# Kernel optimization log

Hardware: AMD Instinct MI355X
Metric: run time of the kernel (lower is better)

## Reference

```python
import jax, jax.numpy as jnp
import numpy as np

NUM_HEADS = 8
NUM_LEVELS = 4
NUM_POINTS = 4
EMBED = 256
HEAD_DIM = EMBED // NUM_HEADS
SPATIAL = [(100, 100), (50, 50), (25, 25), (13, 13)]  # (H, W) per level


def _bilinear_sample(val, grid):
    """torch.nn.functional.grid_sample(mode='bilinear', padding_mode='zeros', align_corners=False).
    val: [B, H, W, C], grid: [B, N, 2] with (x, y) in [-1, 1]. Returns [B, N, C]."""
    B, H, W, C = val.shape
    x = (grid[..., 0] + 1.0) * (W * 0.5) - 0.5
    y = (grid[..., 1] + 1.0) * (H * 0.5) - 0.5
    x0 = jnp.floor(x)
    y0 = jnp.floor(y)
    wx1 = x - x0
    wy1 = y - y0
    wx0 = 1.0 - wx1
    wy0 = 1.0 - wy1
    x0i = x0.astype(jnp.int32)
    y0i = y0.astype(jnp.int32)
    valf = val.reshape(B, H * W, C)

    def corner(xi, yi, w):
        valid = (xi >= 0) & (xi < W) & (yi >= 0) & (yi < H)
        idx = jnp.clip(yi, 0, H - 1) * W + jnp.clip(xi, 0, W - 1)
        v = jnp.take_along_axis(valf, idx[..., None], axis=1)  # [B, N, C]
        return v * (w * valid)[..., None]

    return (corner(x0i, y0i, wx0 * wy0) + corner(x0i + 1, y0i, wx1 * wy0)
            + corner(x0i, y0i + 1, wx0 * wy1) + corner(x0i + 1, y0i + 1, wx1 * wy1))


def setup_inputs() -> dict:
    key = jax.random.key(0)
    ks = jax.random.split(key, 12)
    bs, nq = 4, 6000
    nv = sum(h * w for h, w in SPATIAL)
    s = 0.02
    return {
        "query": jax.random.normal(ks[0], (bs, nq, EMBED), jnp.float32),
        "value": jax.random.normal(ks[1], (bs, nv, EMBED), jnp.float32),
        "reference_points": jax.random.uniform(ks[2], (bs, nq, NUM_LEVELS, 2), jnp.float32),
        "W_off": jax.random.normal(ks[3], (EMBED, NUM_HEADS * NUM_LEVELS * NUM_POINTS * 2), jnp.float32) * s,
        "b_off": jax.random.normal(ks[4], (NUM_HEADS * NUM_LEVELS * NUM_POINTS * 2,), jnp.float32),
        "W_attn": jax.random.normal(ks[5], (EMBED, NUM_HEADS * NUM_LEVELS * NUM_POINTS), jnp.float32) * s,
        "b_attn": jnp.zeros((NUM_HEADS * NUM_LEVELS * NUM_POINTS,), jnp.float32),
        "W_val": jax.random.normal(ks[6], (EMBED, EMBED), jnp.float32) * s,
        "b_val": jnp.zeros((EMBED,), jnp.float32),
        "W_out": jax.random.normal(ks[7], (EMBED, EMBED), jnp.float32) * s,
        "b_out": jnp.zeros((EMBED,), jnp.float32),
        "spatial_shapes": jnp.asarray(np.array(SPATIAL, dtype=np.int32)),
    }


def reference(query, value, reference_points, W_off, b_off, W_attn, b_attn,
              W_val, b_val, W_out, b_out, spatial_shapes):
    shapes = [(int(h), int(w)) for h, w in np.asarray(spatial_shapes)]
    bs, nq, _ = query.shape
    nv = value.shape[1]

    v = (value @ W_val + b_val).reshape(bs, nv, NUM_HEADS, HEAD_DIM)
    offsets = (query @ W_off + b_off).reshape(bs, nq, NUM_HEADS, NUM_LEVELS, NUM_POINTS, 2)
    aw = (query @ W_attn + b_attn).reshape(bs, nq, NUM_HEADS, NUM_LEVELS * NUM_POINTS)
    aw = jax.nn.softmax(aw, axis=-1).reshape(bs, nq, NUM_HEADS, NUM_LEVELS, NUM_POINTS)

    # offset normalizer is [W, H] per level
    norm = jnp.asarray([[w, h] for h, w in shapes], dtype=query.dtype)  # [L, 2]
    loc = reference_points[:, :, None, :, None, :] + offsets / norm[None, None, None, :, None, :]
    grids = 2.0 * loc - 1.0  # [bs, nq, H, L, P, 2]
    # -> [bs*H, nq*P, 2] per level
    grids = jnp.transpose(grids, (0, 2, 1, 3, 4, 5)).reshape(bs * NUM_HEADS, nq, NUM_LEVELS, NUM_POINTS, 2)

    v_bh = jnp.transpose(v, (0, 2, 1, 3)).reshape(bs * NUM_HEADS, nv, HEAD_DIM)
    sampled = []
    start = 0
    for l, (H_, W_) in enumerate(shapes):
        val_l = v_bh[:, start:start + H_ * W_].reshape(bs * NUM_HEADS, H_, W_, HEAD_DIM)
        grid_l = grids[:, :, l].reshape(bs * NUM_HEADS, nq * NUM_POINTS, 2)
        s_l = _bilinear_sample(val_l, grid_l).reshape(bs * NUM_HEADS, nq, NUM_POINTS, HEAD_DIM)
        sampled.append(s_l)
        start += H_ * W_
    sampled = jnp.stack(sampled, axis=2)  # [bs*H, nq, L, P, c]

    aw_bh = jnp.transpose(aw, (0, 2, 1, 3, 4)).reshape(bs * NUM_HEADS, nq, NUM_LEVELS, NUM_POINTS)
    out = (sampled * aw_bh[..., None]).sum(axis=(2, 3))  # [bs*H, nq, c]
    out = out.reshape(bs, NUM_HEADS, nq, HEAD_DIM).transpose(0, 2, 1, 3).reshape(bs, nq, EMBED)
    out = out @ W_out + b_out
    return out + query
```

## Files before the change

kernel.cpp:

```cpp
#include <hip/hip_runtime.h>
#include <hip/hip_bf16.h>

#define BS 4
#define NQ 6000
#define NV 13294
#define NH 8
#define HD 32
#define EMB 256
#define MV (BS * NV)
#define MQ (BS * NQ)

typedef __attribute__((ext_vector_type(8))) short short8;
typedef __attribute__((ext_vector_type(4))) float floatx4;

__device__ __constant__ float LVL_DIM[4] = {100.f, 50.f, 25.f, 13.f};

__device__ inline unsigned short bf16bits(float f) {
  __hip_bfloat16 h = __float2bfloat16(f);
  return *reinterpret_cast<unsigned short*>(&h);
}
__device__ inline float bflo(unsigned int u) { return __uint_as_float(u << 16); }
__device__ inline float bfhi(unsigned int u) { return __uint_as_float(u & 0xffff0000u); }

#define LDS_STRIDE 40

__global__ __launch_bounds__(256) void wtrans_kernel(
    const float* __restrict__ W_val, const float* __restrict__ W_off,
    const float* __restrict__ W_attn, const float* __restrict__ W_out,
    unsigned short* __restrict__ Wt_val, unsigned short* __restrict__ Wt_qcat,
    unsigned short* __restrict__ Wt_out) {
  const int b = blockIdx.x, k = threadIdx.x;
  if (b < 256) {
    Wt_val[b * EMB + k] = bf16bits(W_val[k * 256 + b]);
  } else if (b < 640) {
    const int n = b - 256;
    float v = (n < 256) ? W_off[k * 256 + n] : W_attn[k * 128 + (n - 256)];
    Wt_qcat[n * EMB + k] = bf16bits(v);
  } else {
    const int n = b - 640;
    Wt_out[n * EMB + k] = bf16bits(W_out[k * 256 + n]);
  }
}

__device__ inline void stageA_f32(const float* __restrict__ A, int M, int m0,
                                  int k0, unsigned short* lds, int tid) {
  const int r = tid >> 1, half = tid & 1;
  const int row = m0 + r;
  unsigned short* dst = lds + r * LDS_STRIDE + half * 16;
  if (row < M) {
    const float* src = A + (size_t)row * EMB + k0 + half * 16;
#pragma unroll
    for (int j = 0; j < 4; ++j) {
      float4 v = *(const float4*)(src + 4 * j);
      ushort4 u;
      u.x = bf16bits(v.x);
      u.y = bf16bits(v.y);
      u.z = bf16bits(v.z);
      u.w = bf16bits(v.w);
      *(ushort4*)(dst + 4 * j) = u;
    }
  } else {
    ushort4 z = make_ushort4(0, 0, 0, 0);
#pragma unroll
    for (int j = 0; j < 4; ++j) *(ushort4*)(dst + 4 * j) = z;
  }
}

__device__ inline void stage_bf16(const unsigned short* __restrict__ B, int M,
                                  int n0, int k0, unsigned short* lds, int tid) {
  const int r = tid >> 1, half = tid & 1;
  const int row = n0 + r;
  unsigned short* dst = lds + r * LDS_STRIDE + half * 16;
  if (row < M) {
    const unsigned short* src = B + (size_t)row * EMB + k0 + half * 16;
    uint4 v0 = *(const uint4*)(src);
    uint4 v1 = *(const uint4*)(src + 8);
    *(uint4*)(dst) = v0;
    *(uint4*)(dst + 8) = v1;
  } else {
    uint4 z = make_uint4(0, 0, 0, 0);
    *(uint4*)(dst) = z;
    *(uint4*)(dst + 8) = z;
  }
}

__device__ inline void mfma_step(const unsigned short* ldsA,
                                 const unsigned short* ldsB, int wm, int wn,
                                 int lane, floatx4 acc[4][4]) {
  const unsigned short* ap =
      ldsA + (wm * 64 + (lane & 15)) * LDS_STRIDE + (lane >> 4) * 8;
  const unsigned short* bp =
      ldsB + (wn * 64 + (lane & 15)) * LDS_STRIDE + (lane >> 4) * 8;
  short8 af[4], bfr[4];
#pragma unroll
  for (int t = 0; t < 4; ++t) {
    af[t] = *(const short8*)(ap + t * 16 * LDS_STRIDE);
    bfr[t] = *(const short8*)(bp + t * 16 * LDS_STRIDE);
  }
#pragma unroll
  for (int mt = 0; mt < 4; ++mt)
#pragma unroll
    for (int nt = 0; nt < 4; ++nt)
      acc[mt][nt] = __builtin_amdgcn_mfma_f32_16x16x32_bf16(af[mt], bfr[nt],
                                                            acc[mt][nt], 0, 0, 0);
}

__global__ __launch_bounds__(256) void vproj_kernel(
    const float* __restrict__ value, const unsigned short* __restrict__ Wt,
    const float* __restrict__ b_val, unsigned short* __restrict__ vbh) {
  __shared__ unsigned short ldsA[128 * LDS_STRIDE];
  __shared__ unsigned short ldsB[128 * LDS_STRIDE];
  const int tid = threadIdx.x, lane = tid & 63, w = tid >> 6;
  const int wm = w >> 1, wn = w & 1;
  const int m0 = (blockIdx.x >> 1) * 128;
  const int n0 = (blockIdx.x & 1) * 128;
  floatx4 acc[4][4];
  const floatx4 zero = {0.f, 0.f, 0.f, 0.f};
#pragma unroll
  for (int i = 0; i < 4; i++)
#pragma unroll
    for (int j = 0; j < 4; j++) acc[i][j] = zero;

  for (int k0 = 0; k0 < EMB; k0 += 32) {
    stageA_f32(value, MV, m0, k0, ldsA, tid);
    stage_bf16(Wt, 256, n0, k0, ldsB, tid);
    __syncthreads();
    mfma_step(ldsA, ldsB, wm, wn, lane, acc);
    __syncthreads();
  }

  const int quad = lane >> 4, cl = lane & 15;
#pragma unroll
  for (int mt = 0; mt < 4; ++mt) {
#pragma unroll
    for (int r = 0; r < 4; ++r) {
      const int row = m0 + wm * 64 + mt * 16 + quad * 4 + r;
      if (row < MV) {
        const int b = row / NV, n = row - b * NV;
#pragma unroll
        for (int nt = 0; nt < 4; ++nt) {
          const int c = n0 + wn * 64 + nt * 16 + cl;
          const int h = c >> 5, d = c & 31;
          vbh[(((size_t)(b * NH + h)) * NV + n) * HD + d] =
              bf16bits(acc[mt][nt][r] + b_val[c]);
        }
      }
    }
  }
}

__global__ __launch_bounds__(256) void qproj_kernel(
    const float* __restrict__ query, const unsigned short* __restrict__ Wt,
    const float* __restrict__ refpts, const float* __restrict__ b_off,
    const float* __restrict__ b_attn, float* __restrict__ locbuf,
    float* __restrict__ awbuf) {
  __shared__ unsigned short ldsA[128 * LDS_STRIDE];
  __shared__ unsigned short ldsB[128 * LDS_STRIDE];
  const int tid = threadIdx.x, lane = tid & 63, w = tid >> 6;
  const int wm = w >> 1, wn = w & 1;
  const int m0 = (blockIdx.x / 3) * 128;
  const int n0 = (blockIdx.x % 3) * 128;
  floatx4 acc[4][4];
  const floatx4 zero = {0.f, 0.f, 0.f, 0.f};
#pragma unroll
  for (int i = 0; i < 4; i++)
#pragma unroll
    for (int j = 0; j < 4; j++) acc[i][j] = zero;

  for (int k0 = 0; k0 < EMB; k0 += 32) {
    stageA_f32(query, MQ, m0, k0, ldsA, tid);
    stage_bf16(Wt, 384, n0, k0, ldsB, tid);
    __syncthreads();
    mfma_step(ldsA, ldsB, wm, wn, lane, acc);
    __syncthreads();
  }

  const int quad = lane >> 4, cl = lane & 15;
  if (n0 < 256) {
#pragma unroll
    for (int mt = 0; mt < 4; ++mt) {
#pragma unroll
      for (int r = 0; r < 4; ++r) {
        const int row = m0 + wm * 64 + mt * 16 + quad * 4 + r;
        if (row < MQ) {
#pragma unroll
          for (int nt = 0; nt < 4; ++nt) {
            const int c = n0 + wn * 64 + nt * 16 + cl;
            const int xy = c & 1, l = (c >> 3) & 3;
            const float dim = LVL_DIM[l];
            const float ref = refpts[(size_t)row * 8 + l * 2 + xy];
            locbuf[(size_t)row * 256 + c] =
                ref * dim + acc[mt][nt][r] + b_off[c] - 0.5f;
          }
        }
      }
    }
  } else {
#pragma unroll
    for (int mt = 0; mt < 4; ++mt) {
#pragma unroll
      for (int r = 0; r < 4; ++r) {
        const int row = m0 + wm * 64 + mt * 16 + quad * 4 + r;
        if (row < MQ) {
#pragma unroll
          for (int nt = 0; nt < 4; ++nt) {
            const int ca = wn * 64 + nt * 16 + cl;
            float v = acc[mt][nt][r] + b_attn[ca];
            float m = v;
            m = fmaxf(m, __shfl_xor(m, 1));
            m = fmaxf(m, __shfl_xor(m, 2));
            m = fmaxf(m, __shfl_xor(m, 4));
            m = fmaxf(m, __shfl_xor(m, 8));
            float e = __expf(v - m);
            float s = e;
            s += __shfl_xor(s, 1);
            s += __shfl_xor(s, 2);
            s += __shfl_xor(s, 4);
            s += __shfl_xor(s, 8);
            awbuf[(size_t)row * 128 + ca] = e / s;
          }
        }
      }
    }
  }
}

__global__ __launch_bounds__(256) void sample_kernel(
    const unsigned short* __restrict__ vbh, const float* __restrict__ locbuf,
    const float* __restrict__ awbuf, unsigned short* __restrict__ sampledb) {
  const int wid = (blockIdx.x * 256 + threadIdx.x) >> 6;
  const int lane = threadIdx.x & 63;
  const int h = wid & 7;
  const int row = wid >> 3;
  const int b = row / NQ;
  const unsigned int* vb =
      (const unsigned int*)(vbh) + ((size_t)(b * NH + h)) * NV * 16;
  const int grp = lane >> 4;
  const int d2 = lane & 15;

  const float* locp = locbuf + (size_t)row * 256 + h * 32;
  const float* awp = awbuf + (size_t)row * 128 + h * 16;

  float ax = 0.f, ay = 0.f;
#pragma unroll
  for (int l = 0; l < 4; ++l) {
    const int W_ = (l == 0) ? 100 : (l == 1) ? 50 : (l == 2) ? 25 : 13;
    const int H_ = W_;
    const int START = (l == 0) ? 0 : (l == 1) ? 10000 : (l == 2) ? 12500 : 13125;
    const int s = l * 4 + grp;
    const float2 xy = *(const float2*)(locp + s * 2);
    const float w = awp[s];

    const float fx = floorf(xy.x), fy = floorf(xy.y);
    const int x0 = (int)fx, y0 = (int)fy;
    const float wx1 = xy.x - fx, wy1 = xy.y - fy;
    const float wx0 = 1.f - wx1, wy0 = 1.f - wy1;

    const int x0c = min(max(x0, 0), W_ - 1), x1c = min(max(x0 + 1, 0), W_ - 1);
    const int y0c = min(max(y0, 0), H_ - 1), y1c = min(max(y0 + 1, 0), H_ - 1);
    const float mx0 = (x0 >= 0 && x0 < W_) ? wx0 : 0.f;
    const float mx1 = (x0 + 1 >= 0 && x0 + 1 < W_) ? wx1 : 0.f;
    const float my0 = (y0 >= 0 && y0 < H_) ? wy0 : 0.f;
    const float my1 = (y0 + 1 >= 0 && y0 + 1 < H_) ? wy1 : 0.f;

    const unsigned int* basep = vb + (size_t)START * 16 + d2;
    unsigned int u00 = basep[(y0c * W_ + x0c) * 16];
    unsigned int u01 = basep[(y0c * W_ + x1c) * 16];
    unsigned int u10 = basep[(y1c * W_ + x0c) * 16];
    unsigned int u11 = basep[(y1c * W_ + x1c) * 16];

    const float w00 = w * my0 * mx0, w01 = w * my0 * mx1;
    const float w10 = w * my1 * mx0, w11 = w * my1 * mx1;
    ax += w00 * bflo(u00) + w01 * bflo(u01) + w10 * bflo(u10) + w11 * bflo(u11);
    ay += w00 * bfhi(u00) + w01 * bfhi(u01) + w10 * bfhi(u10) + w11 * bfhi(u11);
  }
  ax += __shfl_xor(ax, 16);
  ax += __shfl_xor(ax, 32);
  ay += __shfl_xor(ay, 16);
  ay += __shfl_xor(ay, 32);
  if (grp == 0) {
    ushort2 o;
    o.x = bf16bits(ax);
    o.y = bf16bits(ay);
    *(ushort2*)(sampledb + (size_t)row * EMB + h * HD + 2 * d2) = o;
  }
}

__global__ __launch_bounds__(256) void oproj_kernel(
    const unsigned short* __restrict__ sampledb,
    const unsigned short* __restrict__ Wt, const float* __restrict__ b_out,
    const float* __restrict__ query, float* __restrict__ out) {
  __shared__ unsigned short ldsA[128 * LDS_STRIDE];
  __shared__ unsigned short ldsB[128 * LDS_STRIDE];
  const int tid = threadIdx.x, lane = tid & 63, w = tid >> 6;
  const int wm = w >> 1, wn = w & 1;
  const int m0 = (blockIdx.x >> 1) * 128;
  const int n0 = (blockIdx.x & 1) * 128;
  floatx4 acc[4][4];
  const floatx4 zero = {0.f, 0.f, 0.f, 0.f};
#pragma unroll
  for (int i = 0; i < 4; i++)
#pragma unroll
    for (int j = 0; j < 4; j++) acc[i][j] = zero;

  for (int k0 = 0; k0 < EMB; k0 += 32) {
    stage_bf16(sampledb, MQ, m0, k0, ldsA, tid);
    stage_bf16(Wt, 256, n0, k0, ldsB, tid);
    __syncthreads();
    mfma_step(ldsA, ldsB, wm, wn, lane, acc);
    __syncthreads();
  }

  const int quad = lane >> 4, cl = lane & 15;
#pragma unroll
  for (int mt = 0; mt < 4; ++mt) {
#pragma unroll
    for (int r = 0; r < 4; ++r) {
      const int row = m0 + wm * 64 + mt * 16 + quad * 4 + r;
      if (row < MQ) {
#pragma unroll
        for (int nt = 0; nt < 4; ++nt) {
          const int c = n0 + wn * 64 + nt * 16 + cl;
          out[(size_t)row * EMB + c] =
              acc[mt][nt][r] + b_out[c] + query[(size_t)row * EMB + c];
        }
      }
    }
  }
}

extern "C" void kernel_launch(void* const* d_in, const int* in_sizes, int n_in,
                              void* d_out, int out_size, void* d_ws,
                              size_t ws_size, hipStream_t stream) {
  const float* query  = (const float*)d_in[0];
  const float* value  = (const float*)d_in[1];
  const float* refpts = (const float*)d_in[2];
  const float* W_off  = (const float*)d_in[3];
  const float* b_off  = (const float*)d_in[4];
  const float* W_attn = (const float*)d_in[5];
  const float* b_attn = (const float*)d_in[6];
  const float* W_val  = (const float*)d_in[7];
  const float* b_val  = (const float*)d_in[8];
  const float* W_out  = (const float*)d_in[9];
  const float* b_out  = (const float*)d_in[10];
  float* out = (float*)d_out;

  char* ws = (char*)d_ws;
  unsigned short* vbh = (unsigned short*)ws;
  float* locbuf = (float*)(ws + 27226112);
  float* awbuf = (float*)(ws + 51802112);
  unsigned short* sampledb = (unsigned short*)(ws + 64090112);
  unsigned short* Wt_val = (unsigned short*)(ws + 76378112);
  unsigned short* Wt_qcat = (unsigned short*)(ws + 76509184);
  unsigned short* Wt_out = (unsigned short*)(ws + 76705792);

  wtrans_kernel<<<896, 256, 0, stream>>>(W_val, W_off, W_attn, W_out, Wt_val,
                                         Wt_qcat, Wt_out);
  vproj_kernel<<<416 * 2, 256, 0, stream>>>(value, Wt_val, b_val, vbh);
  qproj_kernel<<<188 * 3, 256, 0, stream>>>(query, Wt_qcat, refpts, b_off,
                                            b_attn, locbuf, awbuf);
  sample_kernel<<<BS * NQ * NH / 4, 256, 0, stream>>>(vbh, locbuf, awbuf,
                                                      sampledb);
  oproj_kernel<<<188 * 2, 256, 0, stream>>>(sampledb, Wt_out, b_out, query, out);
}
```

Measured before the change: 282.7 us.

## Remap GEMM block order per XCD and vectorize sampling with slice-grouped blocks

The three GEMM kernels now map block IDs so that blocks landing on the same XCD (blockIdx mod 8) share M tiles, which is meant to improve L2 reuse of the A operand. The sample kernel is restructured so each lane handles one sampling point and loads 8 bf16 channels as a uint4, replacing 4 scalar loads per point. It reduces across points with a shuffle tree. Blocks are also ordered so that each XCD works on a fixed set of (batch, head) value slices, keeping the gathered value slice resident in its L2. The cost is more shuffle instructions per wave and padded grids with early-exit blocks in qproj and oproj.

```diff
diff --git a/kernel.cpp b/kernel.cpp
--- a/kernel.cpp
+++ b/kernel.cpp
@@ -112,14 +112,15 @@
   __shared__ unsigned short ldsB[128 * LDS_STRIDE];
   const int tid = threadIdx.x, lane = tid & 63, w = tid >> 6;
   const int wm = w >> 1, wn = w & 1;
-  const int m0 = (blockIdx.x >> 1) * 128;
-  const int n0 = (blockIdx.x & 1) * 128;
+  const int chunk = blockIdx.x >> 4, i = blockIdx.x & 15;
+  const int m0 = (chunk * 8 + (i & 7)) * 128;
+  const int n0 = (i >> 3) * 128;
   floatx4 acc[4][4];
   const floatx4 zero = {0.f, 0.f, 0.f, 0.f};
 #pragma unroll
-  for (int i = 0; i < 4; i++)
-#pragma unroll
-    for (int j = 0; j < 4; j++) acc[i][j] = zero;
+  for (int i2 = 0; i2 < 4; i2++)
+#pragma unroll
+    for (int j = 0; j < 4; j++) acc[i2][j] = zero;
 
   for (int k0 = 0; k0 < EMB; k0 += 32) {
     stageA_f32(value, MV, m0, k0, ldsA, tid);
@@ -158,14 +159,17 @@
   __shared__ unsigned short ldsB[128 * LDS_STRIDE];
   const int tid = threadIdx.x, lane = tid & 63, w = tid >> 6;
   const int wm = w >> 1, wn = w & 1;
-  const int m0 = (blockIdx.x / 3) * 128;
-  const int n0 = (blockIdx.x % 3) * 128;
+  const int chunk = blockIdx.x / 24, i = blockIdx.x % 24;
+  const int m_idx = chunk * 8 + (i & 7);
+  if (m_idx >= 188) return;
+  const int m0 = m_idx * 128;
+  const int n0 = (i >> 3) * 128;
   floatx4 acc[4][4];
   const floatx4 zero = {0.f, 0.f, 0.f, 0.f};
 #pragma unroll
-  for (int i = 0; i < 4; i++)
-#pragma unroll
-    for (int j = 0; j < 4; j++) acc[i][j] = zero;
+  for (int i2 = 0; i2 < 4; i2++)
+#pragma unroll
+    for (int j = 0; j < 4; j++) acc[i2][j] = zero;
 
   for (int k0 = 0; k0 < EMB; k0 += 32) {
     stageA_f32(query, MQ, m0, k0, ldsA, tid);
@@ -228,61 +232,75 @@
 __global__ __launch_bounds__(256) void sample_kernel(
     const unsigned short* __restrict__ vbh, const float* __restrict__ locbuf,
     const float* __restrict__ awbuf, unsigned short* __restrict__ sampledb) {
-  const int wid = (blockIdx.x * 256 + threadIdx.x) >> 6;
+  const int blk = blockIdx.x;
+  const int t = blk >> 3;
+  const int quarter = t / 1500;
+  const int j = t - quarter * 1500;
+  const int slice = (blk & 7) * 4 + quarter;
+  const int h = slice & 7;
+  const int w = threadIdx.x >> 6;
   const int lane = threadIdx.x & 63;
-  const int h = wid & 7;
-  const int row = wid >> 3;
-  const int b = row / NQ;
-  const unsigned int* vb =
-      (const unsigned int*)(vbh) + ((size_t)(b * NH + h)) * NV * 16;
-  const int grp = lane >> 4;
-  const int d2 = lane & 15;
-
-  const float* locp = locbuf + (size_t)row * 256 + h * 32;
-  const float* awp = awbuf + (size_t)row * 128 + h * 16;
-
-  float ax = 0.f, ay = 0.f;
-#pragma unroll
-  for (int l = 0; l < 4; ++l) {
-    const int W_ = (l == 0) ? 100 : (l == 1) ? 50 : (l == 2) ? 25 : 13;
-    const int H_ = W_;
-    const int START = (l == 0) ? 0 : (l == 1) ? 10000 : (l == 2) ? 12500 : 13125;
-    const int s = l * 4 + grp;
-    const float2 xy = *(const float2*)(locp + s * 2);
-    const float w = awp[s];
-
-    const float fx = floorf(xy.x), fy = floorf(xy.y);
-    const int x0 = (int)fx, y0 = (int)fy;
-    const float wx1 = xy.x - fx, wy1 = xy.y - fy;
-    const float wx0 = 1.f - wx1, wy0 = 1.f - wy1;
-
-    const int x0c = min(max(x0, 0), W_ - 1), x1c = min(max(x0 + 1, 0), W_ - 1);
-    const int y0c = min(max(y0, 0), H_ - 1), y1c = min(max(y0 + 1, 0), H_ - 1);
-    const float mx0 = (x0 >= 0 && x0 < W_) ? wx0 : 0.f;
-    const float mx1 = (x0 + 1 >= 0 && x0 + 1 < W_) ? wx1 : 0.f;
-    const float my0 = (y0 >= 0 && y0 < H_) ? wy0 : 0.f;
-    const float my1 = (y0 + 1 >= 0 && y0 + 1 < H_) ? wy1 : 0.f;
-
-    const unsigned int* basep = vb + (size_t)START * 16 + d2;
-    unsigned int u00 = basep[(y0c * W_ + x0c) * 16];
-    unsigned int u01 = basep[(y0c * W_ + x1c) * 16];
-    unsigned int u10 = basep[(y1c * W_ + x0c) * 16];
-    unsigned int u11 = basep[(y1c * W_ + x1c) * 16];
-
-    const float w00 = w * my0 * mx0, w01 = w * my0 * mx1;
-    const float w10 = w * my1 * mx0, w11 = w * my1 * mx1;
-    ax += w00 * bflo(u00) + w01 * bflo(u01) + w10 * bflo(u10) + w11 * bflo(u11);
-    ay += w00 * bfhi(u00) + w01 * bfhi(u01) + w10 * bfhi(u10) + w11 * bfhi(u11);
-  }
-  ax += __shfl_xor(ax, 16);
-  ax += __shfl_xor(ax, 32);
-  ay += __shfl_xor(ay, 16);
-  ay += __shfl_xor(ay, 32);
-  if (grp == 0) {
-    ushort2 o;
-    o.x = bf16bits(ax);
-    o.y = bf16bits(ay);
-    *(ushort2*)(sampledb + (size_t)row * EMB + h * HD + 2 * d2) = o;
+  const int row = (slice >> 3) * NQ + j * 4 + w;
+  const int g = lane >> 2;
+  const int d8 = lane & 3;
+  const int l = g >> 2;
+
+  const int W_ = (l < 2) ? ((l == 0) ? 100 : 50) : ((l == 2) ? 25 : 13);
+  const int START = (l < 2) ? ((l == 0) ? 0 : 10000) : ((l == 2) ? 12500 : 13125);
+
+  const float2 xy = *(const float2*)(locbuf + (size_t)row * 256 + h * 32 + g * 2);
+  const float wgt = awbuf[(size_t)row * 128 + h * 16 + g];
+
+  const float fx = floorf(xy.x), fy = floorf(xy.y);
+  const int x0 = (int)fx, y0 = (int)fy;
+  const float wx1 = xy.x - fx, wy1 = xy.y - fy;
+  const float wx0 = 1.f - wx1, wy0 = 1.f - wy1;
+  const int x0c = min(max(x0, 0), W_ - 1), x1c = min(max(x0 + 1, 0), W_ - 1);
+  const int y0c = min(max(y0, 0), W_ - 1), y1c = min(max(y0 + 1, 0), W_ - 1);
+  const float mx0 = ((unsigned)x0 < (unsigned)W_) ? wx0 : 0.f;
+  const float mx1 = ((unsigned)(x0 + 1) < (unsigned)W_) ? wx1 : 0.f;
+  const float my0 = ((unsigned)y0 < (unsigned)W_) ? wy0 : 0.f;
+  const float my1 = ((unsigned)(y0 + 1) < (unsigned)W_) ? wy1 : 0.f;
+  const float wy0w = wgt * my0, wy1w = wgt * my1;
+  const float w00 = wy0w * mx0, w01 = wy0w * mx1;
+  const float w10 = wy1w * mx0, w11 = wy1w * mx1;
+
+  const unsigned int* base =
+      (const unsigned int*)vbh + ((size_t)slice * NV + START) * 16 + d8 * 4;
+  const int rb0 = y0c * W_, rb1 = y1c * W_;
+  const uint4 u00 = *(const uint4*)(base + (size_t)(rb0 + x0c) * 16);
+  const uint4 u01 = *(const uint4*)(base + (size_t)(rb0 + x1c) * 16);
+  const uint4 u10 = *(const uint4*)(base + (size_t)(rb1 + x0c) * 16);
+  const uint4 u11 = *(const uint4*)(base + (size_t)(rb1 + x1c) * 16);
+
+  float a[8];
+  const unsigned int* p00 = &u00.x;
+  const unsigned int* p01 = &u01.x;
+  const unsigned int* p10 = &u10.x;
+  const unsigned int* p11 = &u11.x;
+#pragma unroll
+  for (int k = 0; k < 4; ++k) {
+    a[2 * k] = w00 * bflo(p00[k]) + w01 * bflo(p01[k]) + w10 * bflo(p10[k]) +
+               w11 * bflo(p11[k]);
+    a[2 * k + 1] = w00 * bfhi(p00[k]) + w01 * bfhi(p01[k]) +
+                   w10 * bfhi(p10[k]) + w11 * bfhi(p11[k]);
+  }
+
+#pragma unroll
+  for (int k = 0; k < 8; ++k) {
+    a[k] += __shfl_xor(a[k], 4);
+    a[k] += __shfl_xor(a[k], 8);
+    a[k] += __shfl_xor(a[k], 16);
+    a[k] += __shfl_xor(a[k], 32);
+  }
+
+  if (g == 0) {
+    uint4 o;
+    o.x = (unsigned)bf16bits(a[0]) | ((unsigned)bf16bits(a[1]) << 16);
+    o.y = (unsigned)bf16bits(a[2]) | ((unsigned)bf16bits(a[3]) << 16);
+    o.z = (unsigned)bf16bits(a[4]) | ((unsigned)bf16bits(a[5]) << 16);
+    o.w = (unsigned)bf16bits(a[6]) | ((unsigned)bf16bits(a[7]) << 16);
+    *(uint4*)(sampledb + (size_t)row * EMB + h * 32 + d8 * 8) = o;
   }
 }
 
@@ -294,14 +312,17 @@
   __shared__ unsigned short ldsB[128 * LDS_STRIDE];
   const int tid = threadIdx.x, lane = tid & 63, w = tid >> 6;
   const int wm = w >> 1, wn = w & 1;
-  const int m0 = (blockIdx.x >> 1) * 128;
-  const int n0 = (blockIdx.x & 1) * 128;
+  const int chunk = blockIdx.x >> 4, i = blockIdx.x & 15;
+  const int m_idx = chunk * 8 + (i & 7);
+  if (m_idx >= 188) return;
+  const int m0 = m_idx * 128;
+  const int n0 = (i >> 3) * 128;
   floatx4 acc[4][4];
   const floatx4 zero = {0.f, 0.f, 0.f, 0.f};
 #pragma unroll
-  for (int i = 0; i < 4; i++)
-#pragma unroll
-    for (int j = 0; j < 4; j++) acc[i][j] = zero;
+  for (int i2 = 0; i2 < 4; i2++)
+#pragma unroll
+    for (int j = 0; j < 4; j++) acc[i2][j] = zero;
 
   for (int k0 = 0; k0 < EMB; k0 += 32) {
     stage_bf16(sampledb, MQ, m0, k0, ldsA, tid);
@@ -356,10 +377,10 @@
 
   wtrans_kernel<<<896, 256, 0, stream>>>(W_val, W_off, W_attn, W_out, Wt_val,
                                          Wt_qcat, Wt_out);
-  vproj_kernel<<<416 * 2, 256, 0, stream>>>(value, Wt_val, b_val, vbh);
-  qproj_kernel<<<188 * 3, 256, 0, stream>>>(query, Wt_qcat, refpts, b_off,
-                                            b_attn, locbuf, awbuf);
+  vproj_kernel<<<832, 256, 0, stream>>>(value, Wt_val, b_val, vbh);
+  qproj_kernel<<<576, 256, 0, stream>>>(query, Wt_qcat, refpts, b_off, b_attn,
+                                        locbuf, awbuf);
   sample_kernel<<<BS * NQ * NH / 4, 256, 0, stream>>>(vbh, locbuf, awbuf,
                                                       sampledb);
-  oproj_kernel<<<188 * 2, 256, 0, stream>>>(sampledb, Wt_out, b_out, query, out);
-}
+  oproj_kernel<<<384, 256, 0, stream>>>(sampledb, Wt_out, b_out, query, out);
+}
```

Measured after the change: 262.5 us. -7.1%, faster.
